# Performance work log

Hardware: AMD Instinct MI355X
Metric: run time of the kernel (lower is better)

## Reference

```python
import jax, jax.numpy as jnp
import numpy as np

N, E, FN, FE, H, L, S = 50000, 800000, 16, 8, 64, 3, 32

def layernorm(h, g, b, eps=1e-5):
    mu = h.mean(-1, keepdims=True)
    var = ((h - mu) ** 2).mean(-1, keepdims=True)
    return (h - mu) / jnp.sqrt(var + eps) * g + b

def setup_inputs() -> dict:
    key = jax.random.key(0)
    ks = iter(jax.random.split(key, 64))
    nrm = lambda shape: jax.random.normal(next(ks), shape, jnp.float32) * 0.05
    inp = {}
    inp['x'] = jax.random.normal(next(ks), (N, FN), jnp.float32)
    inp['edge_index'] = jax.random.randint(next(ks), (2, E), 0, N)
    inp['edge_attr'] = jax.random.normal(next(ks), (E, FE), jnp.float32)
    # node / edge encoders: Linear -> ReLU -> LayerNorm
    inp['Wn'] = nrm((FN, H)); inp['bn'] = jnp.zeros((H,)); inp['gn'] = jnp.ones((H,)); inp['betan'] = jnp.zeros((H,))
    inp['We'] = nrm((FE, H)); inp['be'] = jnp.zeros((H,)); inp['ge'] = jnp.ones((H,)); inp['betae'] = jnp.zeros((H,))
    # EdgeConv MLPs (stacked over layers): Linear(2H,H) -> ReLU -> Linear(H,H)
    inp['Wc1'] = nrm((L, 2 * H, H)); inp['bc1'] = jnp.zeros((L, H))
    inp['Wc2'] = nrm((L, H, H)); inp['bc2'] = jnp.zeros((L, H))
    # GATConv (heads=1): lin weight, att_src, att_dst, bias
    inp['Wg'] = nrm((L, H, H)); inp['att_src'] = nrm((L, H)); inp['att_dst'] = nrm((L, H)); inp['bg'] = jnp.zeros((L, H))
    # q predictor
    inp['Wq1'] = nrm((H, H)); inp['bq1'] = jnp.zeros((H,)); inp['gq'] = jnp.ones((H,)); inp['betaq'] = jnp.zeros((H,))
    inp['Wq2'] = nrm((H, S)); inp['bq2'] = jnp.zeros((S,))
    # value predictor
    inp['Wv1'] = nrm((H, H)); inp['bv1'] = jnp.zeros((H,)); inp['gv'] = jnp.ones((H,)); inp['betav'] = jnp.zeros((H,))
    inp['Wv2'] = nrm((H, 1)); inp['bv2'] = jnp.zeros((1,))
    return inp

def reference(x, edge_index, edge_attr, Wn, bn, gn, betan, We, be, ge, betae,
              Wc1, bc1, Wc2, bc2, Wg, att_src, att_dst, bg,
              Wq1, bq1, gq, betaq, Wq2, bq2, Wv1, bv1, gv, betav, Wv2, bv2):
    n = x.shape[0]
    src, dst = edge_index[0], edge_index[1]  # PyG: row=source(j), col=target(i)
    h = layernorm(jax.nn.relu(x @ Wn + bn), gn, betan)
    _ea = layernorm(jax.nn.relu(edge_attr @ We + be), ge, betae)  # encoded but unused by EdgeConv message (faithful)
    loop = jnp.arange(n)
    gsrc = jnp.concatenate([src, loop])  # GAT adds self-loops
    gdst = jnp.concatenate([dst, loop])
    for l in range(L):
        # EdgeConv: gather x_i (target), x_j (source), concat, MLP, scatter-max at target
        m = jnp.concatenate([h[dst], h[src]], axis=1)  # [E, 2H]
        m = jax.nn.relu(m @ Wc1[l] + bc1[l]) @ Wc2[l] + bc2[l]
        agg = jax.ops.segment_max(m, dst, num_segments=n)
        agg = jnp.where(jnp.isneginf(agg), 0.0, agg)  # PyG scatter-max leaves empty rows at 0
        # GATConv (1 head): alpha = softmax_i(leaky_relu(a_s.xg_j + a_d.xg_i))
        xg = h @ Wg[l]
        a_s = xg @ att_src[l]
        a_d = xg @ att_dst[l]
        e = jax.nn.leaky_relu(a_s[gsrc] + a_d[gdst], 0.2)
        emax = jax.ops.segment_max(e, gdst, num_segments=n)
        w = jnp.exp(e - emax[gdst])
        alpha = w / jax.ops.segment_sum(w, gdst, num_segments=n)[gdst]
        att = jax.ops.segment_sum(xg[gsrc] * alpha[:, None], gdst, num_segments=n) + bg[l]
        h = jax.nn.relu(h + agg + att)
    t = h[0]
    tq = layernorm(jax.nn.relu(t @ Wq1 + bq1), gq, betaq)
    q_values = tq @ Wq2 + bq2
    tv = layernorm(jax.nn.relu(t @ Wv1 + bv1), gv, betav)
    value = tv @ Wv2 + bv2
    return (q_values, value)
```

## Files before the change

kernel.cpp:

```cpp
#include <hip/hip_runtime.h>
#include <math.h>

#define N_NODES 50000
#define N_EDGES 800000
#define FN_DIM 16
#define HD 64
#define T_CAP 8192
#define T2_CAP 512
#define MAXDEG 128

__device__ __forceinline__ float wsum64(float v) {
    #pragma unroll
    for (int o = 1; o < 64; o <<= 1) v += __shfl_xor(v, o);
    return v;
}
__device__ __forceinline__ float wmax64(float v) {
    #pragma unroll
    for (int o = 1; o < 64; o <<= 1) v = fmaxf(v, __shfl_xor(v, o));
    return v;
}
__device__ __forceinline__ float lrelu02(float v) { return v > 0.f ? v : 0.2f * v; }

__global__ void k_zero(int4* __restrict__ p, int n4) {
    int i = blockIdx.x * blockDim.x + threadIdx.x;
    if (i < n4) p[i] = make_int4(0, 0, 0, 0);
}

__global__ void k_mark2(const int* __restrict__ ei, int* need1, int* need2) {
    int e = blockIdx.x * blockDim.x + threadIdx.x;
    if (e == 0) { need1[0] = 1; need2[0] = 1; }
    if (e >= N_EDGES) return;
    if (ei[N_EDGES + e] == 0) { int s = ei[e]; need2[s] = 1; need1[s] = 1; }
}
__global__ void k_mark1(const int* __restrict__ ei, const int* __restrict__ need2, int* need1) {
    int e = blockIdx.x * blockDim.x + threadIdx.x;
    if (e >= N_EDGES) return;
    if (need2[ei[N_EDGES + e]]) need1[ei[e]] = 1;
}
__global__ void k_compact(const int* __restrict__ need1, const int* __restrict__ need2,
                          int* list1, int* list2, int* idx1, int* idx2, int* cnt) {
    int i = blockIdx.x * blockDim.x + threadIdx.x;
    if (i >= N_NODES) return;
    if (need1[i]) { int p = atomicAdd(&cnt[0], 1); if (p < T_CAP)  { list1[p] = i; idx1[i] = p; } }
    if (need2[i]) { int p = atomicAdd(&cnt[1], 1); if (p < T2_CAP) { list2[p] = i; idx2[i] = p; } }
}
__global__ void k_bucket(const int* __restrict__ ei, const int* __restrict__ need1,
                         const int* __restrict__ need2,
                         const int* __restrict__ idx1, const int* __restrict__ idx2,
                         int* eb1, int* deg1, int* eb2, int* deg2, int* eb3, int* deg3) {
    int e = blockIdx.x * blockDim.x + threadIdx.x;
    if (e >= N_EDGES) return;
    int d = ei[N_EDGES + e];
    int s = ei[e];
    if (need1[d]) {
        int t = idx1[d];
        if ((unsigned)t < T_CAP) { int p = atomicAdd(&deg1[t], 1); if (p < MAXDEG) eb1[t * MAXDEG + p] = s; }
    }
    if (need2[d]) {
        int t = idx2[d];
        if ((unsigned)t < T2_CAP) { int p = atomicAdd(&deg2[t], 1); if (p < MAXDEG) eb2[t * MAXDEG + p] = s; }
    }
    if (d == 0) { int p = atomicAdd(deg3, 1); if (p < MAXDEG) eb3[p] = s; }
}

template<int LM>
__device__ __forceinline__ float node_h(int i, int lane,
    const float* __restrict__ x, const float* __restrict__ Wn, const float* __restrict__ bn,
    const float* __restrict__ gn, const float* __restrict__ betan,
    const float* __restrict__ hin) {
    if (LM == 0) {
        float acc = bn[lane];
        #pragma unroll
        for (int k = 0; k < FN_DIM; k++) acc += x[i * FN_DIM + k] * Wn[k * HD + lane];
        float v = fmaxf(acc, 0.f);
        float mu = wsum64(v) * (1.f / 64.f);
        float d = v - mu;
        float var = wsum64(d * d) * (1.f / 64.f);
        return d * rsqrtf(var + 1e-5f) * gn[lane] + betan[lane];
    } else {
        return hin[i * HD + lane];
    }
}

__device__ __forceinline__ void heads_eval(float hv, int lane,
    const float* __restrict__ Wq1, const float* __restrict__ bq1,
    const float* __restrict__ gq, const float* __restrict__ betaq,
    const float* __restrict__ Wq2, const float* __restrict__ bq2,
    const float* __restrict__ Wv1, const float* __restrict__ bv1,
    const float* __restrict__ gv, const float* __restrict__ betav,
    const float* __restrict__ Wv2, const float* __restrict__ bv2,
    float* __restrict__ out) {
    float acc = bq1[lane];
    #pragma unroll 8
    for (int k = 0; k < 64; k++) acc += __shfl(hv, k) * Wq1[k * 64 + lane];
    float r = fmaxf(acc, 0.f);
    float mu = wsum64(r) * (1.f / 64.f);
    float d = r - mu;
    float var = wsum64(d * d) * (1.f / 64.f);
    float tq = d * rsqrtf(var + 1e-5f) * gq[lane] + betaq[lane];
    float accv = bv1[lane];
    #pragma unroll 8
    for (int k = 0; k < 64; k++) accv += __shfl(hv, k) * Wv1[k * 64 + lane];
    float rv = fmaxf(accv, 0.f);
    float muv = wsum64(rv) * (1.f / 64.f);
    float dv = rv - muv;
    float varv = wsum64(dv * dv) * (1.f / 64.f);
    float tv = dv * rsqrtf(varv + 1e-5f) * gv[lane] + betav[lane];
    int s = lane & 31;
    float q = bq2[s];
    #pragma unroll 8
    for (int k = 0; k < 64; k++) q += __shfl(tq, k) * Wq2[k * 32 + s];
    if (lane < 32) out[lane] = q;
    float vsum = wsum64(tv * Wv2[lane]);
    if (lane == 0) out[32] = vsum + bv2[0];
}

template<int LM>
__global__ __launch_bounds__(256) void k_layer(
    const float* __restrict__ x, const float* __restrict__ Wn, const float* __restrict__ bn,
    const float* __restrict__ gn, const float* __restrict__ betan,
    const float* __restrict__ hin,
    const float* __restrict__ Wc1, const float* __restrict__ bc1,
    const float* __restrict__ Wc2, const float* __restrict__ bc2,
    const float* __restrict__ Wg, const float* __restrict__ atts, const float* __restrict__ attd,
    const float* __restrict__ bgv,
    const int* __restrict__ tlist, const int* __restrict__ cntp, int tcap,
    const int* __restrict__ eb, const int* __restrict__ deg,
    float* __restrict__ hout,
    const float* __restrict__ Wq1, const float* __restrict__ bq1,
    const float* __restrict__ gq, const float* __restrict__ betaq,
    const float* __restrict__ Wq2, const float* __restrict__ bq2,
    const float* __restrict__ Wv1, const float* __restrict__ bv1,
    const float* __restrict__ gv, const float* __restrict__ betav,
    const float* __restrict__ Wv2, const float* __restrict__ bv2)
{
    __shared__ float ht[64], ut[64], xgt[64];
    __shared__ float scr[4][4][64];
    __shared__ float xgc[MAXDEG][64];
    __shared__ float ec[MAXDEG];
    __shared__ float redA[4][64], redB[4][64];
    __shared__ float sws[4];
    __shared__ float sA[2];
    __shared__ float sEm;

    int lane = threadIdx.x & 63;
    int wv = threadIdx.x >> 6;
    int ntgt = (LM == 2) ? 1 : min(cntp[0], tcap);

    for (int w = blockIdx.x; w < ntgt; w += gridDim.x) {
        int t = (LM == 2) ? 0 : tlist[w];
        if (wv == 0) {
            float h = node_h<LM>(t, lane, x, Wn, bn, gn, betan, hin);
            ht[lane] = h;
            float u = bc1[lane], xg = 0.f;
            #pragma unroll 4
            for (int k = 0; k < 64; k++) {
                float b = ht[k];
                u  += b * Wc1[k * 64 + lane];
                xg += b * Wg[k * 64 + lane];
            }
            ut[lane] = u; xgt[lane] = xg;
            float a_st = wsum64(xg * atts[lane]);
            float a_dt = wsum64(xg * attd[lane]);
            if (lane == 0) { sA[0] = a_st; sA[1] = a_dt; }
        }
        __syncthreads();
        int dg = deg[(LM == 2) ? 0 : w]; if (dg > MAXDEG) dg = MAXDEG;
        float a_dt = sA[1];
        float aggw = -INFINITY;

        for (int base = wv * 4; base < dg; base += 16) {
            int ne = dg - base; if (ne > 4) ne = 4;
            #pragma unroll
            for (int e = 0; e < 4; e++) {
                if (e < ne) {
                    int s = eb[w * MAXDEG + base + e];
                    scr[wv][e][lane] = node_h<LM>(s, lane, x, Wn, bn, gn, betan, hin);
                }
            }
            float v[4] = {0.f, 0.f, 0.f, 0.f};
            float g[4] = {0.f, 0.f, 0.f, 0.f};
            #pragma unroll 4
            for (int k = 0; k < 64; k++) {
                float wc = Wc1[(64 + k) * 64 + lane];
                float wg = Wg[k * 64 + lane];
                #pragma unroll
                for (int e = 0; e < 4; e++) {
                    float b = scr[wv][e][k];
                    v[e] += b * wc;
                    g[e] += b * wg;
                }
            }
            float ut_l = ut[lane];
            #pragma unroll
            for (int e = 0; e < 4; e++) scr[wv][e][lane] = fmaxf(ut_l + v[e], 0.f);
            float m[4];
            #pragma unroll
            for (int e = 0; e < 4; e++) m[e] = bc2[lane];
            #pragma unroll 4
            for (int k = 0; k < 64; k++) {
                float wc2v = Wc2[k * 64 + lane];
                #pragma unroll
                for (int e = 0; e < 4; e++) m[e] += scr[wv][e][k] * wc2v;
            }
            #pragma unroll
            for (int e = 0; e < 4; e++) {
                if (e < ne) {
                    aggw = fmaxf(aggw, m[e]);
                    int j = base + e;
                    xgc[j][lane] = g[e];
                    float a_ss = wsum64(g[e] * atts[lane]);
                    if (lane == 0) ec[j] = lrelu02(a_ss + a_dt);
                }
            }
        }
        redA[wv][lane] = aggw;
        __syncthreads();

        if (wv == 0) {
            float es = lrelu02(sA[0] + sA[1]);
            float mm = es;
            for (int j = lane; j < dg; j += 64) mm = fmaxf(mm, ec[j]);
            mm = wmax64(mm);
            if (lane == 0) sEm = mm;
        }
        __syncthreads();
        float em = sEm;
        float attv = 0.f, wsv = 0.f;
        for (int j = wv; j < dg; j += 4) {
            float wj = expf(ec[j] - em);
            attv += wj * xgc[j][lane];
            wsv += wj;
        }
        redB[wv][lane] = attv;
        if (lane == 0) sws[wv] = wsv;
        __syncthreads();

        if (wv == 0) {
            float agg = fmaxf(fmaxf(redA[0][lane], redA[1][lane]),
                              fmaxf(redA[2][lane], redA[3][lane]));
            if (dg == 0) agg = 0.f;
            float es = lrelu02(sA[0] + sA[1]);
            float wself = expf(es - em);
            float att = redB[0][lane] + redB[1][lane] + redB[2][lane] + redB[3][lane]
                      + wself * xgt[lane];
            float wsum = sws[0] + sws[1] + sws[2] + sws[3] + wself;
            float hv = fmaxf(ht[lane] + agg + att / wsum + bgv[lane], 0.f);
            if (LM == 2) {
                heads_eval(hv, lane, Wq1, bq1, gq, betaq, Wq2, bq2,
                           Wv1, bv1, gv, betav, Wv2, bv2, hout);
            } else {
                hout[t * HD + lane] = hv;
            }
        }
        __syncthreads();
    }
}

extern "C" void kernel_launch(void* const* d_in, const int* in_sizes, int n_in,
                              void* d_out, int out_size, void* d_ws, size_t ws_size,
                              hipStream_t stream) {
    const float* x        = (const float*)d_in[0];
    const int*   ei       = (const int*)d_in[1];
    const float* Wn       = (const float*)d_in[3];
    const float* bn       = (const float*)d_in[4];
    const float* gn       = (const float*)d_in[5];
    const float* betan    = (const float*)d_in[6];
    const float* Wc1      = (const float*)d_in[11];
    const float* bc1      = (const float*)d_in[12];
    const float* Wc2      = (const float*)d_in[13];
    const float* bc2      = (const float*)d_in[14];
    const float* Wg       = (const float*)d_in[15];
    const float* att_src  = (const float*)d_in[16];
    const float* att_dst  = (const float*)d_in[17];
    const float* bg       = (const float*)d_in[18];
    const float* Wq1      = (const float*)d_in[19];
    const float* bq1      = (const float*)d_in[20];
    const float* gq       = (const float*)d_in[21];
    const float* betaq    = (const float*)d_in[22];
    const float* Wq2      = (const float*)d_in[23];
    const float* bq2      = (const float*)d_in[24];
    const float* Wv1      = (const float*)d_in[25];
    const float* bv1      = (const float*)d_in[26];
    const float* gv       = (const float*)d_in[27];
    const float* betav    = (const float*)d_in[28];
    const float* Wv2      = (const float*)d_in[29];
    const float* bv2      = (const float*)d_in[30];

    float* hB   = (float*)d_ws;
    float* hA   = hB + (size_t)N_NODES * HD;
    int* need1  = (int*)(hA + (size_t)N_NODES * HD);
    int* need2  = need1 + N_NODES;
    int* deg1   = need2 + N_NODES;
    int* deg2   = deg1 + T_CAP;
    int* deg3   = deg2 + T2_CAP;
    int* cnt    = deg3 + 4;
    int* idx1   = cnt + 8;
    int* idx2   = idx1 + N_NODES;
    int* list1  = idx2 + N_NODES;
    int* list2  = list1 + T_CAP;
    int* eb1    = list2 + T2_CAP;
    int* eb2    = eb1 + (size_t)T_CAP * MAXDEG;
    int* eb3    = eb2 + (size_t)T2_CAP * MAXDEG;

    const int zero_ints = 2 * N_NODES + T_CAP + T2_CAP + 12;
    const int n4 = zero_ints / 4;
    const int EB = (N_EDGES + 255) / 256;
    const int NB = (N_NODES + 255) / 256;

    k_zero<<<(n4 + 255) / 256, 256, 0, stream>>>((int4*)need1, n4);
    k_mark2<<<EB, 256, 0, stream>>>(ei, need1, need2);
    k_mark1<<<EB, 256, 0, stream>>>(ei, need2, need1);
    k_compact<<<NB, 256, 0, stream>>>(need1, need2, list1, list2, idx1, idx2, cnt);
    k_bucket<<<EB, 256, 0, stream>>>(ei, need1, need2, idx1, idx2,
                                     eb1, deg1, eb2, deg2, eb3, deg3);

    k_layer<0><<<512, 256, 0, stream>>>(
        x, Wn, bn, gn, betan, (const float*)nullptr,
        Wc1 + 0 * 2 * HD * HD, bc1 + 0 * HD, Wc2 + 0 * HD * HD, bc2 + 0 * HD,
        Wg + 0 * HD * HD, att_src + 0 * HD, att_dst + 0 * HD, bg + 0 * HD,
        list1, cnt + 0, T_CAP, eb1, deg1, hB,
        Wq1, bq1, gq, betaq, Wq2, bq2, Wv1, bv1, gv, betav, Wv2, bv2);

    k_layer<1><<<64, 256, 0, stream>>>(
        x, Wn, bn, gn, betan, hB,
        Wc1 + 1 * 2 * HD * HD, bc1 + 1 * HD, Wc2 + 1 * HD * HD, bc2 + 1 * HD,
        Wg + 1 * HD * HD, att_src + 1 * HD, att_dst + 1 * HD, bg + 1 * HD,
        list2, cnt + 1, T2_CAP, eb2, deg2, hA,
        Wq1, bq1, gq, betaq, Wq2, bq2, Wv1, bv1, gv, betav, Wv2, bv2);

    k_layer<2><<<1, 256, 0, stream>>>(
        x, Wn, bn, gn, betan, hA,
        Wc1 + 2 * 2 * HD * HD, bc1 + 2 * HD, Wc2 + 2 * HD * HD, bc2 + 2 * HD,
        Wg + 2 * HD * HD, att_src + 2 * HD, att_dst + 2 * HD, bg + 2 * HD,
        (const int*)nullptr, cnt + 1, 1, eb3, deg3, (float*)d_out,
        Wq1, bq1, gq, betaq, Wq2, bq2, Wv1, bv1, gv, betav, Wv2, bv2);
}
```

Baseline: 97.61 us.

## Fuse layer kernels into one persistent kernel with grid barriers and merge preprocessing scans

```diff
diff --git a/kernel.cpp b/kernel.cpp
--- a/kernel.cpp
+++ b/kernel.cpp
@@ -8,6 +8,20 @@
 #define T_CAP 8192
 #define T2_CAP 512
 #define MAXDEG 128
+#define LGRID 512
+#define L1BLK 64
+
+struct KP {
+  const float *x; const int *ei;
+  const float *Wn,*bn,*gn,*betan;
+  const float *Wc1,*bc1,*Wc2,*bc2;
+  const float *Wg,*att_s,*att_d,*bg;
+  const float *Wq1,*bq1,*gq,*betaq,*Wq2,*bq2;
+  const float *Wv1,*bv1,*gv,*betav,*Wv2,*bv2;
+  float *out;
+  float *hB,*hA;
+  int *need1,*need2,*deg1,*deg2,*deg3,*cnt,*idx1,*idx2,*list1,*list2,*eb1,*eb2,*eb3;
+};
 
 __device__ __forceinline__ float wsum64(float v) {
     #pragma unroll
@@ -26,114 +40,92 @@
     if (i < n4) p[i] = make_int4(0, 0, 0, 0);
 }
 
-__global__ void k_mark2(const int* __restrict__ ei, int* need1, int* need2) {
+__global__ void k_scanA(const int* __restrict__ ei,
+                        int* need1, int* need2, int* list1, int* list2,
+                        int* idx1, int* idx2, int* cnt, int* eb3, int* deg3) {
     int e = blockIdx.x * blockDim.x + threadIdx.x;
-    if (e == 0) { need1[0] = 1; need2[0] = 1; }
+    if (e == 0) {
+        if (atomicExch(&need2[0], 1) == 0) { int p = atomicAdd(&cnt[1], 1); if (p < T2_CAP) { list2[p] = 0; idx2[0] = p; } }
+        if (atomicExch(&need1[0], 1) == 0) { int p = atomicAdd(&cnt[0], 1); if (p < T_CAP)  { list1[p] = 0; idx1[0] = p; } }
+    }
     if (e >= N_EDGES) return;
-    if (ei[N_EDGES + e] == 0) { int s = ei[e]; need2[s] = 1; need1[s] = 1; }
-}
-__global__ void k_mark1(const int* __restrict__ ei, const int* __restrict__ need2, int* need1) {
-    int e = blockIdx.x * blockDim.x + threadIdx.x;
-    if (e >= N_EDGES) return;
-    if (need2[ei[N_EDGES + e]]) need1[ei[e]] = 1;
-}
-__global__ void k_compact(const int* __restrict__ need1, const int* __restrict__ need2,
-                          int* list1, int* list2, int* idx1, int* idx2, int* cnt) {
-    int i = blockIdx.x * blockDim.x + threadIdx.x;
-    if (i >= N_NODES) return;
-    if (need1[i]) { int p = atomicAdd(&cnt[0], 1); if (p < T_CAP)  { list1[p] = i; idx1[i] = p; } }
-    if (need2[i]) { int p = atomicAdd(&cnt[1], 1); if (p < T2_CAP) { list2[p] = i; idx2[i] = p; } }
-}
-__global__ void k_bucket(const int* __restrict__ ei, const int* __restrict__ need1,
-                         const int* __restrict__ need2,
-                         const int* __restrict__ idx1, const int* __restrict__ idx2,
-                         int* eb1, int* deg1, int* eb2, int* deg2, int* eb3, int* deg3) {
+    if (ei[N_EDGES + e] == 0) {
+        int s = ei[e];
+        int p = atomicAdd(deg3, 1); if (p < MAXDEG) eb3[p] = s;
+        if (atomicExch(&need2[s], 1) == 0) { int q = atomicAdd(&cnt[1], 1); if (q < T2_CAP) { list2[q] = s; idx2[s] = q; } }
+        if (atomicExch(&need1[s], 1) == 0) { int q = atomicAdd(&cnt[0], 1); if (q < T_CAP)  { list1[q] = s; idx1[s] = q; } }
+    }
+}
+
+__global__ void k_scanB(const int* __restrict__ ei, const int* __restrict__ need2,
+                        const int* __restrict__ idx2,
+                        int* need1, int* list1, int* idx1, int* cnt,
+                        int* eb2, int* deg2) {
     int e = blockIdx.x * blockDim.x + threadIdx.x;
     if (e >= N_EDGES) return;
     int d = ei[N_EDGES + e];
-    int s = ei[e];
+    if (need2[d]) {
+        int s = ei[e];
+        unsigned t = (unsigned)idx2[d];
+        if (t < T2_CAP) { int p = atomicAdd(&deg2[t], 1); if (p < MAXDEG) eb2[t * MAXDEG + p] = s; }
+        if (atomicExch(&need1[s], 1) == 0) { int q = atomicAdd(&cnt[0], 1); if (q < T_CAP) { list1[q] = s; idx1[s] = q; } }
+    }
+}
+
+__global__ void k_scanC(const int* __restrict__ ei, const int* __restrict__ need1,
+                        const int* __restrict__ idx1, int* eb1, int* deg1) {
+    int e = blockIdx.x * blockDim.x + threadIdx.x;
+    if (e >= N_EDGES) return;
+    int d = ei[N_EDGES + e];
     if (need1[d]) {
-        int t = idx1[d];
-        if ((unsigned)t < T_CAP) { int p = atomicAdd(&deg1[t], 1); if (p < MAXDEG) eb1[t * MAXDEG + p] = s; }
-    }
-    if (need2[d]) {
-        int t = idx2[d];
-        if ((unsigned)t < T2_CAP) { int p = atomicAdd(&deg2[t], 1); if (p < MAXDEG) eb2[t * MAXDEG + p] = s; }
-    }
-    if (d == 0) { int p = atomicAdd(deg3, 1); if (p < MAXDEG) eb3[p] = s; }
-}
-
-template<int LM>
-__device__ __forceinline__ float node_h(int i, int lane,
-    const float* __restrict__ x, const float* __restrict__ Wn, const float* __restrict__ bn,
-    const float* __restrict__ gn, const float* __restrict__ betan,
-    const float* __restrict__ hin) {
-    if (LM == 0) {
-        float acc = bn[lane];
+        unsigned t = (unsigned)idx1[d];
+        if (t < T_CAP) { int p = atomicAdd(&deg1[t], 1); if (p < MAXDEG) eb1[t * MAXDEG + p] = ei[e]; }
+    }
+}
+
+__device__ __forceinline__ float node_h(int lm, int i, int lane, const KP& p,
+                                        const float* __restrict__ hin) {
+    if (lm == 0) {
+        float acc = p.bn[lane];
         #pragma unroll
-        for (int k = 0; k < FN_DIM; k++) acc += x[i * FN_DIM + k] * Wn[k * HD + lane];
+        for (int k = 0; k < FN_DIM; k++) acc += p.x[i * FN_DIM + k] * p.Wn[k * HD + lane];
         float v = fmaxf(acc, 0.f);
         float mu = wsum64(v) * (1.f / 64.f);
         float d = v - mu;
         float var = wsum64(d * d) * (1.f / 64.f);
-        return d * rsqrtf(var + 1e-5f) * gn[lane] + betan[lane];
+        return d * rsqrtf(var + 1e-5f) * p.gn[lane] + p.betan[lane];
     } else {
-        return hin[i * HD + lane];
-    }
-}
-
-__device__ __forceinline__ void heads_eval(float hv, int lane,
-    const float* __restrict__ Wq1, const float* __restrict__ bq1,
-    const float* __restrict__ gq, const float* __restrict__ betaq,
-    const float* __restrict__ Wq2, const float* __restrict__ bq2,
-    const float* __restrict__ Wv1, const float* __restrict__ bv1,
-    const float* __restrict__ gv, const float* __restrict__ betav,
-    const float* __restrict__ Wv2, const float* __restrict__ bv2,
-    float* __restrict__ out) {
-    float acc = bq1[lane];
+        return hin[(size_t)i * HD + lane];
+    }
+}
+
+__device__ __forceinline__ void heads_eval(float hv, int lane, const KP& p) {
+    float acc = p.bq1[lane];
     #pragma unroll 8
-    for (int k = 0; k < 64; k++) acc += __shfl(hv, k) * Wq1[k * 64 + lane];
+    for (int k = 0; k < 64; k++) acc += __shfl(hv, k) * p.Wq1[k * 64 + lane];
     float r = fmaxf(acc, 0.f);
     float mu = wsum64(r) * (1.f / 64.f);
     float d = r - mu;
     float var = wsum64(d * d) * (1.f / 64.f);
-    float tq = d * rsqrtf(var + 1e-5f) * gq[lane] + betaq[lane];
-    float accv = bv1[lane];
+    float tq = d * rsqrtf(var + 1e-5f) * p.gq[lane] + p.betaq[lane];
+    float accv = p.bv1[lane];
     #pragma unroll 8
-    for (int k = 0; k < 64; k++) accv += __shfl(hv, k) * Wv1[k * 64 + lane];
+    for (int k = 0; k < 64; k++) accv += __shfl(hv, k) * p.Wv1[k * 64 + lane];
     float rv = fmaxf(accv, 0.f);
     float muv = wsum64(rv) * (1.f / 64.f);
     float dv = rv - muv;
     float varv = wsum64(dv * dv) * (1.f / 64.f);
-    float tv = dv * rsqrtf(varv + 1e-5f) * gv[lane] + betav[lane];
+    float tv = dv * rsqrtf(varv + 1e-5f) * p.gv[lane] + p.betav[lane];
     int s = lane & 31;
-    float q = bq2[s];
+    float q = p.bq2[s];
     #pragma unroll 8
-    for (int k = 0; k < 64; k++) q += __shfl(tq, k) * Wq2[k * 32 + s];
-    if (lane < 32) out[lane] = q;
-    float vsum = wsum64(tv * Wv2[lane]);
-    if (lane == 0) out[32] = vsum + bv2[0];
-}
-
-template<int LM>
-__global__ __launch_bounds__(256) void k_layer(
-    const float* __restrict__ x, const float* __restrict__ Wn, const float* __restrict__ bn,
-    const float* __restrict__ gn, const float* __restrict__ betan,
-    const float* __restrict__ hin,
-    const float* __restrict__ Wc1, const float* __restrict__ bc1,
-    const float* __restrict__ Wc2, const float* __restrict__ bc2,
-    const float* __restrict__ Wg, const float* __restrict__ atts, const float* __restrict__ attd,
-    const float* __restrict__ bgv,
-    const int* __restrict__ tlist, const int* __restrict__ cntp, int tcap,
-    const int* __restrict__ eb, const int* __restrict__ deg,
-    float* __restrict__ hout,
-    const float* __restrict__ Wq1, const float* __restrict__ bq1,
-    const float* __restrict__ gq, const float* __restrict__ betaq,
-    const float* __restrict__ Wq2, const float* __restrict__ bq2,
-    const float* __restrict__ Wv1, const float* __restrict__ bv1,
-    const float* __restrict__ gv, const float* __restrict__ betav,
-    const float* __restrict__ Wv2, const float* __restrict__ bv2)
-{
+    for (int k = 0; k < 64; k++) q += __shfl(tq, k) * p.Wq2[k * 32 + s];
+    if (lane < 32) p.out[lane] = q;
+    float vsum = wsum64(tv * p.Wv2[lane]);
+    if (lane == 0) p.out[32] = vsum + p.bv2[0];
+}
+
+__global__ __launch_bounds__(256) void k_layers(KP p) {
     __shared__ float ht[64], ut[64], xgt[64];
     __shared__ float scr[4][4][64];
     __shared__ float xgc[MAXDEG][64];
@@ -143,196 +135,213 @@
     __shared__ float sA[2];
     __shared__ float sEm;
 
-    int lane = threadIdx.x & 63;
-    int wv = threadIdx.x >> 6;
-    int ntgt = (LM == 2) ? 1 : min(cntp[0], tcap);
-
-    for (int w = blockIdx.x; w < ntgt; w += gridDim.x) {
-        int t = (LM == 2) ? 0 : tlist[w];
-        if (wv == 0) {
-            float h = node_h<LM>(t, lane, x, Wn, bn, gn, betan, hin);
-            ht[lane] = h;
-            float u = bc1[lane], xg = 0.f;
-            #pragma unroll 4
-            for (int k = 0; k < 64; k++) {
-                float b = ht[k];
-                u  += b * Wc1[k * 64 + lane];
-                xg += b * Wg[k * 64 + lane];
-            }
-            ut[lane] = u; xgt[lane] = xg;
-            float a_st = wsum64(xg * atts[lane]);
-            float a_dt = wsum64(xg * attd[lane]);
-            if (lane == 0) { sA[0] = a_st; sA[1] = a_dt; }
-        }
-        __syncthreads();
-        int dg = deg[(LM == 2) ? 0 : w]; if (dg > MAXDEG) dg = MAXDEG;
-        float a_dt = sA[1];
-        float aggw = -INFINITY;
-
-        for (int base = wv * 4; base < dg; base += 16) {
-            int ne = dg - base; if (ne > 4) ne = 4;
-            #pragma unroll
-            for (int e = 0; e < 4; e++) {
-                if (e < ne) {
-                    int s = eb[w * MAXDEG + base + e];
-                    scr[wv][e][lane] = node_h<LM>(s, lane, x, Wn, bn, gn, betan, hin);
-                }
-            }
-            float v[4] = {0.f, 0.f, 0.f, 0.f};
-            float g[4] = {0.f, 0.f, 0.f, 0.f};
-            #pragma unroll 4
-            for (int k = 0; k < 64; k++) {
-                float wc = Wc1[(64 + k) * 64 + lane];
-                float wg = Wg[k * 64 + lane];
+    const int tid = threadIdx.x;
+    const int lane = tid & 63;
+    const int wv = tid >> 6;
+    const int bid = blockIdx.x;
+
+    for (int lm = 0; lm < 3; lm++) {
+        int ntgt, stride;
+        const int *tl, *ebp, *dgp;
+        const float *hin;
+        float *hout;
+        const float *Wc1l = p.Wc1 + lm * 2 * HD * HD, *bc1l = p.bc1 + lm * HD;
+        const float *Wc2l = p.Wc2 + lm * HD * HD,     *bc2l = p.bc2 + lm * HD;
+        const float *Wgl  = p.Wg  + lm * HD * HD,     *bgl  = p.bg  + lm * HD;
+        const float *attsl = p.att_s + lm * HD, *attdl = p.att_d + lm * HD;
+        if (lm == 0)      { ntgt = min(p.cnt[0], T_CAP);  tl = p.list1; ebp = p.eb1; dgp = p.deg1; hin = p.hA; hout = p.hB; stride = gridDim.x; }
+        else if (lm == 1) { ntgt = min(p.cnt[1], T2_CAP); tl = p.list2; ebp = p.eb2; dgp = p.deg2; hin = p.hB; hout = p.hA; stride = L1BLK; }
+        else              { ntgt = 1;                     tl = nullptr; ebp = p.eb3; dgp = p.deg3; hin = p.hA; hout = p.out; stride = 1; }
+
+        for (int w = bid; w < ntgt; w += stride) {
+            int t = (lm == 2) ? 0 : tl[w];
+            const int* row = ebp + (size_t)((lm == 2) ? 0 : w) * MAXDEG;
+            if (wv == 0) {
+                float h = node_h(lm, t, lane, p, hin);
+                ht[lane] = h;
+                float u = bc1l[lane], xg = 0.f;
+                #pragma unroll 4
+                for (int k = 0; k < 64; k++) {
+                    float b = ht[k];
+                    u  += b * Wc1l[k * 64 + lane];
+                    xg += b * Wgl[k * 64 + lane];
+                }
+                ut[lane] = u; xgt[lane] = xg;
+                float a_st = wsum64(xg * attsl[lane]);
+                float a_dt = wsum64(xg * attdl[lane]);
+                if (lane == 0) { sA[0] = a_st; sA[1] = a_dt; }
+            }
+            __syncthreads();
+            int dg = dgp[(lm == 2) ? 0 : w]; if (dg > MAXDEG) dg = MAXDEG;
+            float a_dt = sA[1];
+            float aggw = -INFINITY;
+
+            for (int base = wv * 4; base < dg; base += 16) {
+                int ne = dg - base; if (ne > 4) ne = 4;
                 #pragma unroll
                 for (int e = 0; e < 4; e++) {
-                    float b = scr[wv][e][k];
-                    v[e] += b * wc;
-                    g[e] += b * wg;
-                }
-            }
-            float ut_l = ut[lane];
-            #pragma unroll
-            for (int e = 0; e < 4; e++) scr[wv][e][lane] = fmaxf(ut_l + v[e], 0.f);
-            float m[4];
-            #pragma unroll
-            for (int e = 0; e < 4; e++) m[e] = bc2[lane];
-            #pragma unroll 4
-            for (int k = 0; k < 64; k++) {
-                float wc2v = Wc2[k * 64 + lane];
+                    if (e < ne) {
+                        int s = row[base + e];
+                        scr[wv][e][lane] = node_h(lm, s, lane, p, hin);
+                    }
+                }
+                float v[4] = {0.f, 0.f, 0.f, 0.f};
+                float g[4] = {0.f, 0.f, 0.f, 0.f};
+                #pragma unroll 4
+                for (int k = 0; k < 64; k++) {
+                    float wc = Wc1l[(64 + k) * 64 + lane];
+                    float wg = Wgl[k * 64 + lane];
+                    #pragma unroll
+                    for (int e = 0; e < 4; e++) {
+                        float b = scr[wv][e][k];
+                        v[e] += b * wc;
+                        g[e] += b * wg;
+                    }
+                }
+                float ut_l = ut[lane];
                 #pragma unroll
-                for (int e = 0; e < 4; e++) m[e] += scr[wv][e][k] * wc2v;
-            }
-            #pragma unroll
-            for (int e = 0; e < 4; e++) {
-                if (e < ne) {
-                    aggw = fmaxf(aggw, m[e]);
-                    int j = base + e;
-                    xgc[j][lane] = g[e];
-                    float a_ss = wsum64(g[e] * atts[lane]);
-                    if (lane == 0) ec[j] = lrelu02(a_ss + a_dt);
-                }
-            }
+                for (int e = 0; e < 4; e++) scr[wv][e][lane] = fmaxf(ut_l + v[e], 0.f);
+                float m[4];
+                #pragma unroll
+                for (int e = 0; e < 4; e++) m[e] = bc2l[lane];
+                #pragma unroll 4
+                for (int k = 0; k < 64; k++) {
+                    float wc2v = Wc2l[k * 64 + lane];
+                    #pragma unroll
+                    for (int e = 0; e < 4; e++) m[e] += scr[wv][e][k] * wc2v;
+                }
+                #pragma unroll
+                for (int e = 0; e < 4; e++) {
+                    if (e < ne) {
+                        aggw = fmaxf(aggw, m[e]);
+                        int j = base + e;
+                        xgc[j][lane] = g[e];
+                        float a_ss = wsum64(g[e] * attsl[lane]);
+                        if (lane == 0) ec[j] = lrelu02(a_ss + a_dt);
+                    }
+                }
+            }
+            redA[wv][lane] = aggw;
+            __syncthreads();
+
+            if (wv == 0) {
+                float es = lrelu02(sA[0] + sA[1]);
+                float mm = es;
+                for (int j = lane; j < dg; j += 64) mm = fmaxf(mm, ec[j]);
+                mm = wmax64(mm);
+                if (lane == 0) sEm = mm;
+            }
+            __syncthreads();
+            float em = sEm;
+            float attv = 0.f, wsv = 0.f;
+            for (int j = wv; j < dg; j += 4) {
+                float wj = expf(ec[j] - em);
+                attv += wj * xgc[j][lane];
+                wsv += wj;
+            }
+            redB[wv][lane] = attv;
+            if (lane == 0) sws[wv] = wsv;
+            __syncthreads();
+
+            if (wv == 0) {
+                float agg = fmaxf(fmaxf(redA[0][lane], redA[1][lane]),
+                                  fmaxf(redA[2][lane], redA[3][lane]));
+                if (dg == 0) agg = 0.f;
+                float es = lrelu02(sA[0] + sA[1]);
+                float wself = expf(es - em);
+                float att = redB[0][lane] + redB[1][lane] + redB[2][lane] + redB[3][lane]
+                          + wself * xgt[lane];
+                float wsum = sws[0] + sws[1] + sws[2] + sws[3] + wself;
+                float hv = fmaxf(ht[lane] + agg + att / wsum + bgl[lane], 0.f);
+                if (lm == 2) heads_eval(hv, lane, p);
+                else hout[(size_t)t * HD + lane] = hv;
+            }
+            __syncthreads();
         }
-        redA[wv][lane] = aggw;
-        __syncthreads();
-
-        if (wv == 0) {
-            float es = lrelu02(sA[0] + sA[1]);
-            float mm = es;
-            for (int j = lane; j < dg; j += 64) mm = fmaxf(mm, ec[j]);
-            mm = wmax64(mm);
-            if (lane == 0) sEm = mm;
+
+        if (lm == 0) {
+            __builtin_amdgcn_fence(__ATOMIC_RELEASE, "agent");
+            __syncthreads();
+            if (tid == 0) atomicAdd(&p.cnt[2], 1);
+            if (bid >= L1BLK) return;
+            if (tid == 0) {
+                while (__hip_atomic_load(&p.cnt[2], __ATOMIC_RELAXED, __HIP_MEMORY_SCOPE_AGENT) < (int)gridDim.x)
+                    __builtin_amdgcn_s_sleep(8);
+            }
+            __syncthreads();
+            __builtin_amdgcn_fence(__ATOMIC_ACQUIRE, "agent");
+        } else if (lm == 1) {
+            __builtin_amdgcn_fence(__ATOMIC_RELEASE, "agent");
+            __syncthreads();
+            if (tid == 0) atomicAdd(&p.cnt[3], 1);
+            if (bid != 0) return;
+            if (tid == 0) {
+                while (__hip_atomic_load(&p.cnt[3], __ATOMIC_RELAXED, __HIP_MEMORY_SCOPE_AGENT) < L1BLK)
+                    __builtin_amdgcn_s_sleep(8);
+            }
+            __syncthreads();
+            __builtin_amdgcn_fence(__ATOMIC_ACQUIRE, "agent");
         }
-        __syncthreads();
-        float em = sEm;
-        float attv = 0.f, wsv = 0.f;
-        for (int j = wv; j < dg; j += 4) {
-            float wj = expf(ec[j] - em);
-            attv += wj * xgc[j][lane];
-            wsv += wj;
-        }
-        redB[wv][lane] = attv;
-        if (lane == 0) sws[wv] = wsv;
-        __syncthreads();
-
-        if (wv == 0) {
-            float agg = fmaxf(fmaxf(redA[0][lane], redA[1][lane]),
-                              fmaxf(redA[2][lane], redA[3][lane]));
-            if (dg == 0) agg = 0.f;
-            float es = lrelu02(sA[0] + sA[1]);
-            float wself = expf(es - em);
-            float att = redB[0][lane] + redB[1][lane] + redB[2][lane] + redB[3][lane]
-                      + wself * xgt[lane];
-            float wsum = sws[0] + sws[1] + sws[2] + sws[3] + wself;
-            float hv = fmaxf(ht[lane] + agg + att / wsum + bgv[lane], 0.f);
-            if (LM == 2) {
-                heads_eval(hv, lane, Wq1, bq1, gq, betaq, Wq2, bq2,
-                           Wv1, bv1, gv, betav, Wv2, bv2, hout);
-            } else {
-                hout[t * HD + lane] = hv;
-            }
-        }
-        __syncthreads();
     }
 }
 
 extern "C" void kernel_launch(void* const* d_in, const int* in_sizes, int n_in,
                               void* d_out, int out_size, void* d_ws, size_t ws_size,
                               hipStream_t stream) {
-    const float* x        = (const float*)d_in[0];
-    const int*   ei       = (const int*)d_in[1];
-    const float* Wn       = (const float*)d_in[3];
-    const float* bn       = (const float*)d_in[4];
-    const float* gn       = (const float*)d_in[5];
-    const float* betan    = (const float*)d_in[6];
-    const float* Wc1      = (const float*)d_in[11];
-    const float* bc1      = (const float*)d_in[12];
-    const float* Wc2      = (const float*)d_in[13];
-    const float* bc2      = (const float*)d_in[14];
-    const float* Wg       = (const float*)d_in[15];
-    const float* att_src  = (const float*)d_in[16];
-    const float* att_dst  = (const float*)d_in[17];
-    const float* bg       = (const float*)d_in[18];
-    const float* Wq1      = (const float*)d_in[19];
-    const float* bq1      = (const float*)d_in[20];
-    const float* gq       = (const float*)d_in[21];
-    const float* betaq    = (const float*)d_in[22];
-    const float* Wq2      = (const float*)d_in[23];
-    const float* bq2      = (const float*)d_in[24];
-    const float* Wv1      = (const float*)d_in[25];
-    const float* bv1      = (const float*)d_in[26];
-    const float* gv       = (const float*)d_in[27];
-    const float* betav    = (const float*)d_in[28];
-    const float* Wv2      = (const float*)d_in[29];
-    const float* bv2      = (const float*)d_in[30];
-
-    float* hB   = (float*)d_ws;
-    float* hA   = hB + (size_t)N_NODES * HD;
-    int* need1  = (int*)(hA + (size_t)N_NODES * HD);
-    int* need2  = need1 + N_NODES;
-    int* deg1   = need2 + N_NODES;
-    int* deg2   = deg1 + T_CAP;
-    int* deg3   = deg2 + T2_CAP;
-    int* cnt    = deg3 + 4;
-    int* idx1   = cnt + 8;
-    int* idx2   = idx1 + N_NODES;
-    int* list1  = idx2 + N_NODES;
-    int* list2  = list1 + T_CAP;
-    int* eb1    = list2 + T2_CAP;
-    int* eb2    = eb1 + (size_t)T_CAP * MAXDEG;
-    int* eb3    = eb2 + (size_t)T2_CAP * MAXDEG;
+    KP p;
+    p.x      = (const float*)d_in[0];
+    p.ei     = (const int*)d_in[1];
+    p.Wn     = (const float*)d_in[3];
+    p.bn     = (const float*)d_in[4];
+    p.gn     = (const float*)d_in[5];
+    p.betan  = (const float*)d_in[6];
+    p.Wc1    = (const float*)d_in[11];
+    p.bc1    = (const float*)d_in[12];
+    p.Wc2    = (const float*)d_in[13];
+    p.bc2    = (const float*)d_in[14];
+    p.Wg     = (const float*)d_in[15];
+    p.att_s  = (const float*)d_in[16];
+    p.att_d  = (const float*)d_in[17];
+    p.bg     = (const float*)d_in[18];
+    p.Wq1    = (const float*)d_in[19];
+    p.bq1    = (const float*)d_in[20];
+    p.gq     = (const float*)d_in[21];
+    p.betaq  = (const float*)d_in[22];
+    p.Wq2    = (const float*)d_in[23];
+    p.bq2    = (const float*)d_in[24];
+    p.Wv1    = (const float*)d_in[25];
+    p.bv1    = (const float*)d_in[26];
+    p.gv     = (const float*)d_in[27];
+    p.betav  = (const float*)d_in[28];
+    p.Wv2    = (const float*)d_in[29];
+    p.bv2    = (const float*)d_in[30];
+    p.out    = (float*)d_out;
+
+    p.hB    = (float*)d_ws;
+    p.hA    = p.hB + (size_t)N_NODES * HD;
+    p.need1 = (int*)(p.hA + (size_t)N_NODES * HD);
+    p.need2 = p.need1 + N_NODES;
+    p.deg1  = p.need2 + N_NODES;
+    p.deg2  = p.deg1 + T_CAP;
+    p.deg3  = p.deg2 + T2_CAP;
+    p.cnt   = p.deg3 + 4;
+    p.idx1  = p.cnt + 8;
+    p.idx2  = p.idx1 + N_NODES;
+    p.list1 = p.idx2 + N_NODES;
+    p.list2 = p.list1 + T_CAP;
+    p.eb1   = p.list2 + T2_CAP;
+    p.eb2   = p.eb1 + (size_t)T_CAP * MAXDEG;
+    p.eb3   = p.eb2 + (size_t)T2_CAP * MAXDEG;
 
     const int zero_ints = 2 * N_NODES + T_CAP + T2_CAP + 12;
     const int n4 = zero_ints / 4;
     const int EB = (N_EDGES + 255) / 256;
-    const int NB = (N_NODES + 255) / 256;
-
-    k_zero<<<(n4 + 255) / 256, 256, 0, stream>>>((int4*)need1, n4);
-    k_mark2<<<EB, 256, 0, stream>>>(ei, need1, need2);
-    k_mark1<<<EB, 256, 0, stream>>>(ei, need2, need1);
-    k_compact<<<NB, 256, 0, stream>>>(need1, need2, list1, list2, idx1, idx2, cnt);
-    k_bucket<<<EB, 256, 0, stream>>>(ei, need1, need2, idx1, idx2,
-                                     eb1, deg1, eb2, deg2, eb3, deg3);
-
-    k_layer<0><<<512, 256, 0, stream>>>(
-        x, Wn, bn, gn, betan, (const float*)nullptr,
-        Wc1 + 0 * 2 * HD * HD, bc1 + 0 * HD, Wc2 + 0 * HD * HD, bc2 + 0 * HD,
-        Wg + 0 * HD * HD, att_src + 0 * HD, att_dst + 0 * HD, bg + 0 * HD,
-        list1, cnt + 0, T_CAP, eb1, deg1, hB,
-        Wq1, bq1, gq, betaq, Wq2, bq2, Wv1, bv1, gv, betav, Wv2, bv2);
-
-    k_layer<1><<<64, 256, 0, stream>>>(
-        x, Wn, bn, gn, betan, hB,
-        Wc1 + 1 * 2 * HD * HD, bc1 + 1 * HD, Wc2 + 1 * HD * HD, bc2 + 1 * HD,
-        Wg + 1 * HD * HD, att_src + 1 * HD, att_dst + 1 * HD, bg + 1 * HD,
-        list2, cnt + 1, T2_CAP, eb2, deg2, hA,
-        Wq1, bq1, gq, betaq, Wq2, bq2, Wv1, bv1, gv, betav, Wv2, bv2);
-
-    k_layer<2><<<1, 256, 0, stream>>>(
-        x, Wn, bn, gn, betan, hA,
-        Wc1 + 2 * 2 * HD * HD, bc1 + 2 * HD, Wc2 + 2 * HD * HD, bc2 + 2 * HD,
-        Wg + 2 * HD * HD, att_src + 2 * HD, att_dst + 2 * HD, bg + 2 * HD,
-        (const int*)nullptr, cnt + 1, 1, eb3, deg3, (float*)d_out,
-        Wq1, bq1, gq, betaq, Wq2, bq2, Wv1, bv1, gv, betav, Wv2, bv2);
-}
+
+    k_zero<<<(n4 + 255) / 256, 256, 0, stream>>>((int4*)p.need1, n4);
+    k_scanA<<<EB, 256, 0, stream>>>(p.ei, p.need1, p.need2, p.list1, p.list2,
+                                    p.idx1, p.idx2, p.cnt, p.eb3, p.deg3);
+    k_scanB<<<EB, 256, 0, stream>>>(p.ei, p.need2, p.idx2,
+                                    p.need1, p.list1, p.idx1, p.cnt, p.eb2, p.deg2);
+    k_scanC<<<EB, 256, 0, stream>>>(p.ei, p.need1, p.idx1, p.eb1, p.deg1);
+    k_layers<<<LGRID, 256, 0, stream>>>(p);
+}
```

Result: slower. 138.6 us (+42.0%).

## Fuse frontier marking, compaction and bucketing into three edge scans

Applied to the files above, without the earlier changes.

```diff
diff --git a/kernel.cpp b/kernel.cpp
--- a/kernel.cpp
+++ b/kernel.cpp
@@ -26,41 +26,47 @@
     if (i < n4) p[i] = make_int4(0, 0, 0, 0);
 }
 
-__global__ void k_mark2(const int* __restrict__ ei, int* need1, int* need2) {
+__global__ void k_scanA(const int* __restrict__ ei,
+                        int* need1, int* need2, int* list1, int* list2,
+                        int* idx1, int* idx2, int* cnt, int* eb3, int* deg3) {
     int e = blockIdx.x * blockDim.x + threadIdx.x;
-    if (e == 0) { need1[0] = 1; need2[0] = 1; }
+    if (e == 0) {
+        if (atomicExch(&need2[0], 1) == 0) { int p = atomicAdd(&cnt[1], 1); if (p < T2_CAP) { list2[p] = 0; idx2[0] = p; } }
+        if (atomicExch(&need1[0], 1) == 0) { int p = atomicAdd(&cnt[0], 1); if (p < T_CAP)  { list1[p] = 0; idx1[0] = p; } }
+    }
     if (e >= N_EDGES) return;
-    if (ei[N_EDGES + e] == 0) { int s = ei[e]; need2[s] = 1; need1[s] = 1; }
-}
-__global__ void k_mark1(const int* __restrict__ ei, const int* __restrict__ need2, int* need1) {
-    int e = blockIdx.x * blockDim.x + threadIdx.x;
-    if (e >= N_EDGES) return;
-    if (need2[ei[N_EDGES + e]]) need1[ei[e]] = 1;
-}
-__global__ void k_compact(const int* __restrict__ need1, const int* __restrict__ need2,
-                          int* list1, int* list2, int* idx1, int* idx2, int* cnt) {
-    int i = blockIdx.x * blockDim.x + threadIdx.x;
-    if (i >= N_NODES) return;
-    if (need1[i]) { int p = atomicAdd(&cnt[0], 1); if (p < T_CAP)  { list1[p] = i; idx1[i] = p; } }
-    if (need2[i]) { int p = atomicAdd(&cnt[1], 1); if (p < T2_CAP) { list2[p] = i; idx2[i] = p; } }
-}
-__global__ void k_bucket(const int* __restrict__ ei, const int* __restrict__ need1,
-                         const int* __restrict__ need2,
-                         const int* __restrict__ idx1, const int* __restrict__ idx2,
-                         int* eb1, int* deg1, int* eb2, int* deg2, int* eb3, int* deg3) {
+    if (ei[N_EDGES + e] == 0) {
+        int s = ei[e];
+        int p = atomicAdd(deg3, 1); if (p < MAXDEG) eb3[p] = s;
+        if (atomicExch(&need2[s], 1) == 0) { int q = atomicAdd(&cnt[1], 1); if (q < T2_CAP) { list2[q] = s; idx2[s] = q; } }
+        if (atomicExch(&need1[s], 1) == 0) { int q = atomicAdd(&cnt[0], 1); if (q < T_CAP)  { list1[q] = s; idx1[s] = q; } }
+    }
+}
+
+__global__ void k_scanB(const int* __restrict__ ei, const int* __restrict__ need2,
+                        const int* __restrict__ idx2,
+                        int* need1, int* list1, int* idx1, int* cnt,
+                        int* eb2, int* deg2) {
     int e = blockIdx.x * blockDim.x + threadIdx.x;
     if (e >= N_EDGES) return;
     int d = ei[N_EDGES + e];
-    int s = ei[e];
+    if (need2[d]) {
+        int s = ei[e];
+        unsigned t = (unsigned)idx2[d];
+        if (t < T2_CAP) { int p = atomicAdd(&deg2[t], 1); if (p < MAXDEG) eb2[t * MAXDEG + p] = s; }
+        if (atomicExch(&need1[s], 1) == 0) { int q = atomicAdd(&cnt[0], 1); if (q < T_CAP) { list1[q] = s; idx1[s] = q; } }
+    }
+}
+
+__global__ void k_scanC(const int* __restrict__ ei, const int* __restrict__ need1,
+                        const int* __restrict__ idx1, int* eb1, int* deg1) {
+    int e = blockIdx.x * blockDim.x + threadIdx.x;
+    if (e >= N_EDGES) return;
+    int d = ei[N_EDGES + e];
     if (need1[d]) {
-        int t = idx1[d];
-        if ((unsigned)t < T_CAP) { int p = atomicAdd(&deg1[t], 1); if (p < MAXDEG) eb1[t * MAXDEG + p] = s; }
-    }
-    if (need2[d]) {
-        int t = idx2[d];
-        if ((unsigned)t < T2_CAP) { int p = atomicAdd(&deg2[t], 1); if (p < MAXDEG) eb2[t * MAXDEG + p] = s; }
-    }
-    if (d == 0) { int p = atomicAdd(deg3, 1); if (p < MAXDEG) eb3[p] = s; }
+        unsigned t = (unsigned)idx1[d];
+        if (t < T_CAP) { int p = atomicAdd(&deg1[t], 1); if (p < MAXDEG) eb1[t * MAXDEG + p] = ei[e]; }
+    }
 }
 
 template<int LM>
@@ -306,14 +312,13 @@
     const int zero_ints = 2 * N_NODES + T_CAP + T2_CAP + 12;
     const int n4 = zero_ints / 4;
     const int EB = (N_EDGES + 255) / 256;
-    const int NB = (N_NODES + 255) / 256;
 
     k_zero<<<(n4 + 255) / 256, 256, 0, stream>>>((int4*)need1, n4);
-    k_mark2<<<EB, 256, 0, stream>>>(ei, need1, need2);
-    k_mark1<<<EB, 256, 0, stream>>>(ei, need2, need1);
-    k_compact<<<NB, 256, 0, stream>>>(need1, need2, list1, list2, idx1, idx2, cnt);
-    k_bucket<<<EB, 256, 0, stream>>>(ei, need1, need2, idx1, idx2,
-                                     eb1, deg1, eb2, deg2, eb3, deg3);
+    k_scanA<<<EB, 256, 0, stream>>>(ei, need1, need2, list1, list2,
+                                    idx1, idx2, cnt, eb3, deg3);
+    k_scanB<<<EB, 256, 0, stream>>>(ei, need2, idx2,
+                                    need1, list1, idx1, cnt, eb2, deg2);
+    k_scanC<<<EB, 256, 0, stream>>>(ei, need1, idx1, eb1, deg1);
 
     k_layer<0><<<512, 256, 0, stream>>>(
         x, Wn, bn, gn, betan, (const float*)nullptr,
```

New measurement: 96.96 us. No clear change (-0.7%).
